# Kernel tuning notes

Hardware: AMD Instinct MI355X
Metric: run time of the kernel (lower is better)

Reference implementation:

```python
import jax, jax.numpy as jnp
import numpy as np

B, N, F_IN, T = 8, 325, 32, 24
H, C = 4, 32  # num_heads, out_channels
K = 3         # k_neighbors


def _build_graph(seed=0):
    rng = np.random.default_rng(seed)
    dist = rng.uniform(0.1, 1.0, size=(N, N)).astype(np.float32)
    np.fill_diagonal(dist, 0.0)
    # per-row: k nearest among strictly-positive distances
    masked = np.where(dist > 0, dist, np.inf)
    idx = np.argsort(masked, axis=1)[:, :K]           # (N, K)
    rows = np.arange(N)[:, None]
    nd = dist[rows, idx]                              # (N, K)
    w = 1.0 / (nd + 1e-6)
    w = w / (w.sum(axis=1, keepdims=True) + 1e-6)
    adj_mask = np.zeros((N, N), np.float32)
    init_w = np.zeros((N, N), np.float32)
    adj_mask[rows, idx] = 1.0
    init_w[rows, idx] = w
    return adj_mask, init_w


def setup_inputs() -> dict:
    key = jax.random.key(0)
    k1, k2, k3, k4 = jax.random.split(key, 4)
    adj_mask, init_w = _build_graph()
    x = jax.random.normal(k1, (B, N, F_IN, T), dtype=jnp.float32)
    W_w = jax.random.normal(k2, (H * C, F_IN), dtype=jnp.float32) * (1.0 / np.sqrt(F_IN))
    W_b = jnp.zeros((H * C,), dtype=jnp.float32)
    attn_w = jax.random.normal(k3, (H, 2 * C), dtype=jnp.float32) * (1.0 / np.sqrt(2 * C))
    return {
        "x": x,
        "W_w": W_w,
        "W_b": W_b,
        "attn_w": attn_w,
        "initial_weights": jnp.asarray(init_w),
        "initial_weights_base": jnp.asarray(init_w),
        "adj_mask": jnp.asarray(adj_mask),
    }


def _constrain(w, base, adj_mask):
    w = jnp.clip(w, base * 0.5, base * 1.5)
    w = jnp.maximum(w, 0.0)
    s = jnp.sum(w * adj_mask, axis=1, keepdims=True)
    s = s + (s == 0).astype(w.dtype) * 1e-6
    return w * adj_mask / s


def reference(x, W_w, W_b, attn_w, initial_weights, initial_weights_base, adj_mask):
    b, n, f_in, t = x.shape
    xp = jnp.transpose(x, (0, 3, 1, 2))                    # (B,T,N,F)
    Wh = (xp @ W_w.T + W_b).reshape(b, t, n, H, C)         # (B,T,N,H,C)
    w = _constrain(initial_weights, initial_weights_base, adj_mask)
    a1, a2 = attn_w[:, :C], attn_w[:, C:]
    # attn(cat[Wh_i, Wh_j]) == Wh_i.a1 + Wh_j.a2 (no bias)
    f1 = jnp.einsum('btnhc,hc->btnh', Wh, a1)
    f2 = jnp.einsum('btnhc,hc->btnh', Wh, a2)
    e = f1[:, :, :, None, :] + f2[:, :, None, :, :]        # (B,T,N,N,H)
    score = jax.nn.leaky_relu(e, negative_slope=0.2)
    score = score * adj_mask[None, None, :, :, None] + w[None, None, :, :, None]
    attention = jax.nn.softmax(score, axis=3)              # softmax over j (includes zeroed non-edges, as in torch)
    out = jnp.einsum('btijh,btjhc->btihc', attention, Wh).reshape(b, t, n, H * C)
    return jnp.transpose(out, (0, 2, 3, 1))                # (B,N,H*C,T)
```

## Files before the change

kernel.cpp:

```cpp
#include <hip/hip_runtime.h>
#include <math.h>

#define Bq 8
#define Nq 325
#define F_INq 32
#define Tq 24
#define HCq 128
#define KMAX 4

__global__ __launch_bounds__(192) void prep_kernel(
    const float* __restrict__ iw, const float* __restrict__ ib,
    const float* __restrict__ adj, const float* __restrict__ Ww,
    const float* __restrict__ Wb, const float* __restrict__ attnw,
    const float* __restrict__ x,
    int* __restrict__ nbr_cnt, int* __restrict__ nbr_idx, float* __restrict__ nbr_w,
    float* __restrict__ WxT, float* __restrict__ Wp,
    float* __restrict__ bx, float* __restrict__ xp) {
  int blk = blockIdx.x;
  int tid = threadIdx.x;
  if (blk < Nq) {
    if (tid >= 64) return;
    int lane = tid;
    int i = blk;
    const float* iwr = iw + (size_t)i * Nq;
    const float* ibr = ib + (size_t)i * Nq;
    const float* ar  = adj + (size_t)i * Nq;
    float wa_c[6], a_c[6];
    float sum = 0.f;
    #pragma unroll
    for (int c = 0; c < 6; ++c) {
      int j = c * 64 + lane;
      float wa = 0.f, a = 0.f;
      if (j < Nq) {
        float basev = ibr[j];
        float w = iwr[j];
        w = fminf(fmaxf(w, basev * 0.5f), basev * 1.5f);
        w = fmaxf(w, 0.f);
        a = ar[j];
        wa = w * a;
      }
      wa_c[c] = wa; a_c[c] = a;
      sum += wa;
    }
    #pragma unroll
    for (int off = 32; off >= 1; off >>= 1) sum += __shfl_xor(sum, off, 64);
    if (sum == 0.f) sum = 1e-6f;
    float inv = 1.f / sum;
    unsigned long long below = (1ull << lane) - 1ull;
    int base = 0;
    #pragma unroll
    for (int c = 0; c < 6; ++c) {
      int j = c * 64 + lane;
      bool pred = (j < Nq) && (a_c[c] != 0.f);
      unsigned long long m = __ballot(pred);
      int rank = base + __popcll(m & below);
      if (pred && rank < KMAX) {
        nbr_idx[i * KMAX + rank] = j;
        nbr_w[i * KMAX + rank]   = wa_c[c] * inv;
      }
      base += __popcll(m);
    }
    if (lane == 0) {
      int cnt = base < KMAX ? base : KMAX;
      for (int k = cnt; k < KMAX; ++k) { nbr_idx[i * KMAX + k] = 0; nbr_w[i * KMAX + k] = 0.f; }
      nbr_cnt[i] = cnt;
    }
    return;
  }
  if (blk == Nq) {
    for (int o = tid; o < F_INq * HCq; o += 192) {
      int f = o >> 7, r = o & 127;
      WxT[o] = Ww[r * F_INq + f];
    }
    for (int o = tid; o < 8 * F_INq; o += 192) {
      int p = o >> 5, f = o & 31;
      int h = p & 3, c0 = (p < 4) ? 0 : 32;
      float v = 0.f;
      for (int c = 0; c < 32; ++c)
        v += Ww[(h * 32 + c) * F_INq + f] * attnw[h * 64 + c0 + c];
      Wp[o] = v;
    }
    for (int r = tid; r < 136; r += 192) {
      float v;
      if (r < HCq) {
        v = Wb[r];
      } else {
        int h = (r - HCq) & 3, c0 = (r < 132) ? 0 : 32;
        v = 0.f;
        for (int c = 0; c < 32; ++c) v += Wb[h * 32 + c] * attnw[h * 64 + c0 + c];
      }
      bx[r] = v;
    }
    return;
  }
  {
    int pblk = blk - (Nq + 1);
    int b = pblk / 13, c = pblk - b * 13;
    const float4* src = (const float4*)x + ((size_t)b * Nq + c * 25) * 192;
    float4 a = {0.f, 0.f, 0.f, 0.f};
    #pragma unroll 5
    for (int n = 0; n < 25; ++n) {
      float4 v = src[(size_t)n * 192 + tid];
      a.x += v.x; a.y += v.y; a.z += v.z; a.w += v.w;
    }
    ((float4*)xp)[(size_t)pblk * 192 + tid] = a;
  }
}

__global__ __launch_bounds__(256) void fused_kernel(
    const float* __restrict__ x, const float* __restrict__ Wp,
    const float* __restrict__ WxT, const float* __restrict__ bx,
    const float* __restrict__ xp,
    const int* __restrict__ nbr_cnt, const int* __restrict__ nbr_idx,
    const float* __restrict__ nbr_w, float* __restrict__ out) {
  __shared__ __align__(16) float sx[6144];
  __shared__ __align__(16) float sxs[768];
  __shared__ __align__(16) float spd[2][3][96];
  __shared__ float sbp[2][96], sps[2][96];
  __shared__ float ssw[2][3];
  __shared__ int ssi[2][3], scnt2[2];
  int tid = threadIdx.x;
  int blk = blockIdx.x;
  int b = blk / 163;
  int i0 = (blk - b * 163) * 2;
  int valid1 = (i0 + 1 < Nq) ? 1 : 0;
  if (tid < 2) {
    int i = i0 + (tid & valid1);
    int c = nbr_cnt[i];
    scnt2[tid] = c < 3 ? c : 3;
  }
  if (tid < 6) {
    int ii = tid / 3, k = tid - ii * 3;
    int i = i0 + (ii & valid1);
    ssi[ii][k] = nbr_idx[i * KMAX + k];
    ssw[ii][k] = nbr_w[i * KMAX + k];
  }
  __syncthreads();
  const float4* x4 = (const float4*)x;
  float4* sx4 = (float4*)sx;
  #pragma unroll
  for (int j = 0; j < 6; ++j) {
    int idx = tid + j * 256;
    int slot = idx / 192, e4 = idx - slot * 192;
    int ii = slot >> 2, sl = slot & 3;
    int node = (sl == 0) ? (i0 + (ii & valid1)) : ssi[ii][sl - 1];
    sx4[idx] = x4[((size_t)(b * Nq + node)) * 192 + e4];
  }
  if (tid < 192) {
    const float4* xpb = (const float4*)xp + (size_t)b * 13 * 192;
    float4 a = {0.f, 0.f, 0.f, 0.f};
    #pragma unroll
    for (int c = 0; c < 13; ++c) {
      float4 v = xpb[c * 192 + tid];
      a.x += v.x; a.y += v.y; a.z += v.z; a.w += v.w;
    }
    ((float4*)sxs)[tid] = a;
  }
  __syncthreads();
  if (tid < 192) {
    int ii = tid / 96, r96 = tid - ii * 96;
    int h = r96 / 24, t = r96 - h * 24;
    const float* xi  = sx + (ii * 4 + 0) * 768 + t;
    const float* xj0 = sx + (ii * 4 + 1) * 768 + t;
    const float* xj1 = sx + (ii * 4 + 2) * 768 + t;
    const float* xj2 = sx + (ii * 4 + 3) * 768 + t;
    const float* w1 = Wp + h * 32;
    const float* w2 = Wp + (4 + h) * 32;
    float f1 = bx[128 + h], g0 = bx[132 + h], g1 = g0, g2 = g0;
    #pragma unroll
    for (int f = 0; f < 32; ++f) {
      float wa = w1[f], wb2 = w2[f];
      f1 += wa * xi[f * 24];
      g0 += wb2 * xj0[f * 24];
      g1 += wb2 * xj1[f * 24];
      g2 += wb2 * xj2[f * 24];
    }
    int cnt = scnt2[ii];
    float fv[3] = {g0, g1, g2};
    float sv[3];
    float m = 0.f;
    #pragma unroll
    for (int k = 0; k < 3; ++k) {
      float s = 0.f;
      if (k < cnt) {
        float e = f1 + fv[k];
        e = e > 0.f ? e : 0.2f * e;
        s = e + ssw[ii][k];
        m = fmaxf(m, s);
      }
      sv[k] = s;
    }
    float em = __expf(-m);
    float Z = (float)(Nq - cnt) * em;
    float pk[3];
    #pragma unroll
    for (int k = 0; k < 3; ++k) {
      float p = 0.f;
      if (k < cnt) { p = __expf(sv[k] - m); Z += p; }
      pk[k] = p;
    }
    float invZ = 1.f / Z;
    float bp = em * invZ;
    float ps = 0.f;
    sbp[ii][r96] = bp;
    #pragma unroll
    for (int k = 0; k < 3; ++k) {
      float pd = (k < cnt) ? pk[k] * invZ - bp : 0.f;
      spd[ii][k][r96] = pd;
      ps += pd;
    }
    sps[ii][r96] = ps;
  }
  __syncthreads();
  int lane = tid & 63;
  int w = __builtin_amdgcn_readfirstlane(tid >> 6);
  int ii = lane / 24, t = lane - ii * 24;
  bool act = (lane < 48);
  float acc[32];
  if (act) {
    int ht = w * 24 + t;
    float bpv = sbp[ii][ht];
    float psv = sps[ii][ht];
    float p0 = spd[ii][0][ht], p1 = spd[ii][1][ht], p2 = spd[ii][2][ht];
    float initc = psv + 325.f * bpv;
    const float* bxp = bx + w * 32;
    #pragma unroll
    for (int r = 0; r < 32; ++r) acc[r] = initc * bxp[r];
    const float* xj0 = sx + (ii * 4 + 1) * 768 + t;
    const float* xj1 = sx + (ii * 4 + 2) * 768 + t;
    const float* xj2 = sx + (ii * 4 + 3) * 768 + t;
    const float* xsp = sxs + t;
    const float* wtp = WxT + w * 32;
    #pragma unroll 4
    for (int f = 0; f < 32; ++f) {
      float yv = p0 * xj0[f * 24] + p1 * xj1[f * 24] + p2 * xj2[f * 24]
               + bpv * xsp[f * 24];
      const float* wr = wtp + f * 128;
      #pragma unroll
      for (int r = 0; r < 32; ++r) acc[r] += wr[r] * yv;
    }
  }
  __syncthreads();
  if (act) {
    float* otp = sx + ii * 3072 + (w * 32) * 24 + t;
    #pragma unroll
    for (int r = 0; r < 32; ++r) otp[r * 24] = acc[r];
  }
  __syncthreads();
  float4* o4 = (float4*)(out + ((size_t)(b * Nq + i0)) * 3072);
  int lim = valid1 ? 1536 : 768;
  #pragma unroll
  for (int j = 0; j < 6; ++j) {
    int idx = tid + j * 256;
    if (idx < lim) o4[idx] = sx4[idx];
  }
}

extern "C" void kernel_launch(void* const* d_in, const int* in_sizes, int n_in,
                              void* d_out, int out_size, void* d_ws, size_t ws_size,
                              hipStream_t stream) {
  const float* x     = (const float*)d_in[0];
  const float* Ww    = (const float*)d_in[1];
  const float* Wb    = (const float*)d_in[2];
  const float* attnw = (const float*)d_in[3];
  const float* iw    = (const float*)d_in[4];
  const float* ib    = (const float*)d_in[5];
  const float* adj   = (const float*)d_in[6];
  float* out = (float*)d_out;

  float* ws = (float*)d_ws;
  float* xp  = ws;
  float* WxT = xp + (size_t)Bq * 13 * 768;
  float* Wp  = WxT + F_INq * HCq;
  float* bx  = Wp + 8 * F_INq;
  int* nbr_cnt = (int*)(bx + 136);
  int* nbr_idx = nbr_cnt + Nq;
  float* nbr_w = (float*)(nbr_idx + Nq * KMAX);

  prep_kernel<<<Nq + 1 + Bq * 13, 192, 0, stream>>>(
      iw, ib, adj, Ww, Wb, attnw, x,
      nbr_cnt, nbr_idx, nbr_w, WxT, Wp, bx, xp);
  fused_kernel<<<Bq * 163, 256, 0, stream>>>(x, Wp, WxT, bx, xp,
                                             nbr_cnt, nbr_idx, nbr_w, out);
}
```

Baseline: 104.5 us.

## Restructure output projection so each thread owns one channel across all timesteps

The final projection is remapped so that each thread holds one row of W in registers and accumulates all 24 timesteps for one node. The aggregated input yv is precomputed into shared memory by the softmax threads. Output is written directly as contiguous float4s instead of being staged through shared memory, and the transposed weight buffer WxT is dropped. The neighbour prep now packs three rows per 192-thread block instead of using one wave per block. The cost is more shared memory per block (an extra 24KB yv buffer), which may reduce occupancy.

```diff
diff --git a/kernel.cpp b/kernel.cpp
--- a/kernel.cpp
+++ b/kernel.cpp
@@ -7,6 +7,7 @@
 #define Tq 24
 #define HCq 128
 #define KMAX 4
+#define NBN 109
 
 __global__ __launch_bounds__(192) void prep_kernel(
     const float* __restrict__ iw, const float* __restrict__ ib,
@@ -14,14 +15,13 @@
     const float* __restrict__ Wb, const float* __restrict__ attnw,
     const float* __restrict__ x,
     int* __restrict__ nbr_cnt, int* __restrict__ nbr_idx, float* __restrict__ nbr_w,
-    float* __restrict__ WxT, float* __restrict__ Wp,
-    float* __restrict__ bx, float* __restrict__ xp) {
+    float* __restrict__ Wp, float* __restrict__ bx, float* __restrict__ xp) {
   int blk = blockIdx.x;
   int tid = threadIdx.x;
-  if (blk < Nq) {
-    if (tid >= 64) return;
-    int lane = tid;
-    int i = blk;
+  if (blk < NBN) {
+    int lane = tid & 63;
+    int i = blk * 3 + (tid >> 6);
+    if (i >= Nq) return;
     const float* iwr = iw + (size_t)i * Nq;
     const float* ibr = ib + (size_t)i * Nq;
     const float* ar  = adj + (size_t)i * Nq;
@@ -67,11 +67,7 @@
     }
     return;
   }
-  if (blk == Nq) {
-    for (int o = tid; o < F_INq * HCq; o += 192) {
-      int f = o >> 7, r = o & 127;
-      WxT[o] = Ww[r * F_INq + f];
-    }
+  if (blk == NBN) {
     for (int o = tid; o < 8 * F_INq; o += 192) {
       int p = o >> 5, f = o & 31;
       int h = p & 3, c0 = (p < 4) ? 0 : 32;
@@ -94,7 +90,7 @@
     return;
   }
   {
-    int pblk = blk - (Nq + 1);
+    int pblk = blk - (NBN + 1);
     int b = pblk / 13, c = pblk - b * 13;
     const float4* src = (const float4*)x + ((size_t)b * Nq + c * 25) * 192;
     float4 a = {0.f, 0.f, 0.f, 0.f};
@@ -109,14 +105,14 @@
 
 __global__ __launch_bounds__(256) void fused_kernel(
     const float* __restrict__ x, const float* __restrict__ Wp,
-    const float* __restrict__ WxT, const float* __restrict__ bx,
+    const float* __restrict__ Ww, const float* __restrict__ bx,
     const float* __restrict__ xp,
     const int* __restrict__ nbr_cnt, const int* __restrict__ nbr_idx,
     const float* __restrict__ nbr_w, float* __restrict__ out) {
   __shared__ __align__(16) float sx[6144];
   __shared__ __align__(16) float sxs[768];
-  __shared__ __align__(16) float spd[2][3][96];
-  __shared__ float sbp[2][96], sps[2][96];
+  __shared__ __align__(16) float syv[6144];
+  __shared__ __align__(16) float sinit[192];
   __shared__ float ssw[2][3];
   __shared__ int ssi[2][3], scnt2[2];
   int tid = threadIdx.x;
@@ -124,10 +120,26 @@
   int b = blk / 163;
   int i0 = (blk - b * 163) * 2;
   int valid1 = (i0 + 1 < Nq) ? 1 : 0;
+
+  int lane = tid & 63;
+  int h = tid >> 6;
+  int gii = lane >> 5, c = lane & 31;
+  int r = h * 32 + c;
+  float wr_[32];
+  {
+    const float4* wwp = (const float4*)(Ww + r * 32);
+    #pragma unroll
+    for (int q = 0; q < 8; ++q) {
+      float4 v = wwp[q];
+      wr_[4 * q] = v.x; wr_[4 * q + 1] = v.y; wr_[4 * q + 2] = v.z; wr_[4 * q + 3] = v.w;
+    }
+  }
+  float bxv = bx[r];
+
   if (tid < 2) {
     int i = i0 + (tid & valid1);
-    int c = nbr_cnt[i];
-    scnt2[tid] = c < 3 ? c : 3;
+    int cc = nbr_cnt[i];
+    scnt2[tid] = cc < 3 ? cc : 3;
   }
   if (tid < 6) {
     int ii = tid / 3, k = tid - ii * 3;
@@ -150,8 +162,8 @@
     const float4* xpb = (const float4*)xp + (size_t)b * 13 * 192;
     float4 a = {0.f, 0.f, 0.f, 0.f};
     #pragma unroll
-    for (int c = 0; c < 13; ++c) {
-      float4 v = xpb[c * 192 + tid];
+    for (int cc = 0; cc < 13; ++cc) {
+      float4 v = xpb[cc * 192 + tid];
       a.x += v.x; a.y += v.y; a.z += v.z; a.w += v.w;
     }
     ((float4*)sxs)[tid] = a;
@@ -159,14 +171,14 @@
   __syncthreads();
   if (tid < 192) {
     int ii = tid / 96, r96 = tid - ii * 96;
-    int h = r96 / 24, t = r96 - h * 24;
+    int th = r96 / 24, t = r96 - th * 24;
     const float* xi  = sx + (ii * 4 + 0) * 768 + t;
     const float* xj0 = sx + (ii * 4 + 1) * 768 + t;
     const float* xj1 = sx + (ii * 4 + 2) * 768 + t;
     const float* xj2 = sx + (ii * 4 + 3) * 768 + t;
-    const float* w1 = Wp + h * 32;
-    const float* w2 = Wp + (4 + h) * 32;
-    float f1 = bx[128 + h], g0 = bx[132 + h], g1 = g0, g2 = g0;
+    const float* w1 = Wp + th * 32;
+    const float* w2 = Wp + (4 + th) * 32;
+    float f1 = bx[128 + th], g0 = bx[132 + th], g1 = g0, g2 = g0;
     #pragma unroll
     for (int f = 0; f < 32; ++f) {
       float wa = w1[f], wb2 = w2[f];
@@ -201,58 +213,43 @@
     }
     float invZ = 1.f / Z;
     float bp = em * invZ;
-    float ps = 0.f;
-    sbp[ii][r96] = bp;
-    #pragma unroll
-    for (int k = 0; k < 3; ++k) {
-      float pd = (k < cnt) ? pk[k] * invZ - bp : 0.f;
-      spd[ii][k][r96] = pd;
-      ps += pd;
-    }
-    sps[ii][r96] = ps;
+    float pd0 = (0 < cnt) ? pk[0] * invZ - bp : 0.f;
+    float pd1 = (1 < cnt) ? pk[1] * invZ - bp : 0.f;
+    float pd2 = (2 < cnt) ? pk[2] * invZ - bp : 0.f;
+    float ps = pd0 + pd1 + pd2;
+    sinit[(ii * 4 + th) * 24 + t] = ps + 325.f * bp;
+    float* yvw = syv + (ii * 4 + th) * 768 + t;
+    const float* xsp = sxs + t;
+    #pragma unroll
+    for (int f = 0; f < 32; ++f) {
+      yvw[f * 24] = pd0 * xj0[f * 24] + pd1 * xj1[f * 24] + pd2 * xj2[f * 24]
+                  + bp * xsp[f * 24];
+    }
   }
   __syncthreads();
-  int lane = tid & 63;
-  int w = __builtin_amdgcn_readfirstlane(tid >> 6);
-  int ii = lane / 24, t = lane - ii * 24;
-  bool act = (lane < 48);
-  float acc[32];
-  if (act) {
-    int ht = w * 24 + t;
-    float bpv = sbp[ii][ht];
-    float psv = sps[ii][ht];
-    float p0 = spd[ii][0][ht], p1 = spd[ii][1][ht], p2 = spd[ii][2][ht];
-    float initc = psv + 325.f * bpv;
-    const float* bxp = bx + w * 32;
-    #pragma unroll
-    for (int r = 0; r < 32; ++r) acc[r] = initc * bxp[r];
-    const float* xj0 = sx + (ii * 4 + 1) * 768 + t;
-    const float* xj1 = sx + (ii * 4 + 2) * 768 + t;
-    const float* xj2 = sx + (ii * 4 + 3) * 768 + t;
-    const float* xsp = sxs + t;
-    const float* wtp = WxT + w * 32;
+  float acc[24];
+  {
+    const float* sip = sinit + (gii * 4 + h) * 24;
+    #pragma unroll
+    for (int t = 0; t < 24; ++t) acc[t] = sip[t] * bxv;
+    const float* yvp = syv + (gii * 4 + h) * 768;
     #pragma unroll 4
     for (int f = 0; f < 32; ++f) {
-      float yv = p0 * xj0[f * 24] + p1 * xj1[f * 24] + p2 * xj2[f * 24]
-               + bpv * xsp[f * 24];
-      const float* wr = wtp + f * 128;
+      const float* yf = yvp + f * 24;
+      float wv = wr_[f];
       #pragma unroll
-      for (int r = 0; r < 32; ++r) acc[r] += wr[r] * yv;
-    }
-  }
-  __syncthreads();
-  if (act) {
-    float* otp = sx + ii * 3072 + (w * 32) * 24 + t;
-    #pragma unroll
-    for (int r = 0; r < 32; ++r) otp[r * 24] = acc[r];
-  }
-  __syncthreads();
-  float4* o4 = (float4*)(out + ((size_t)(b * Nq + i0)) * 3072);
-  int lim = valid1 ? 1536 : 768;
-  #pragma unroll
-  for (int j = 0; j < 6; ++j) {
-    int idx = tid + j * 256;
-    if (idx < lim) o4[idx] = sx4[idx];
+      for (int t = 0; t < 24; ++t) acc[t] += wv * yf[t];
+    }
+  }
+  int node = i0 + gii;
+  if (node < Nq) {
+    float4* op4 = (float4*)(out + ((size_t)(b * Nq + node) * HCq + r) * Tq);
+    #pragma unroll
+    for (int q = 0; q < 6; ++q) {
+      float4 v;
+      v.x = acc[4 * q]; v.y = acc[4 * q + 1]; v.z = acc[4 * q + 2]; v.w = acc[4 * q + 3];
+      op4[q] = v;
+    }
   }
 }
 
@@ -270,16 +267,15 @@
 
   float* ws = (float*)d_ws;
   float* xp  = ws;
-  float* WxT = xp + (size_t)Bq * 13 * 768;
-  float* Wp  = WxT + F_INq * HCq;
+  float* Wp  = xp + (size_t)Bq * 13 * 768;
   float* bx  = Wp + 8 * F_INq;
   int* nbr_cnt = (int*)(bx + 136);
   int* nbr_idx = nbr_cnt + Nq;
   float* nbr_w = (float*)(nbr_idx + Nq * KMAX);
 
-  prep_kernel<<<Nq + 1 + Bq * 13, 192, 0, stream>>>(
+  prep_kernel<<<NBN + 1 + Bq * 13, 192, 0, stream>>>(
       iw, ib, adj, Ww, Wb, attnw, x,
-      nbr_cnt, nbr_idx, nbr_w, WxT, Wp, bx, xp);
-  fused_kernel<<<Bq * 163, 256, 0, stream>>>(x, Wp, WxT, bx, xp,
+      nbr_cnt, nbr_idx, nbr_w, Wp, bx, xp);
+  fused_kernel<<<Bq * 163, 256, 0, stream>>>(x, Wp, Ww, bx, xp,
                                              nbr_cnt, nbr_idx, nbr_w, out);
 }
```

Result: slower. 111.5 us (+6.7%).
